# Optimization experiments

Hardware: AMD Instinct MI355X
Metric: run time of the kernel (lower is better)

## Reference

```python
import jax, jax.numpy as jnp
import numpy as np

C_Z = 128
C_H = 128
L = 512
EPS = 1e-5


def _layer_norm(x, w, b):
    mu = jnp.mean(x, axis=-1, keepdims=True)
    var = jnp.mean(jnp.square(x - mu), axis=-1, keepdims=True)
    return (x - mu) * jax.lax.rsqrt(var + EPS) * w + b


def setup_inputs() -> dict:
    key = jax.random.key(0)
    ks = jax.random.split(key, 10)
    s_z = 1.0 / np.sqrt(C_Z)
    s_h = 1.0 / np.sqrt(C_H)
    return {
        "z": jax.random.normal(ks[0], (L, L, C_Z), dtype=jnp.float32),
        "pair_mask": jax.random.randint(ks[1], (L, L), 0, 2, dtype=jnp.int32),
        "ln_in_w": jnp.ones((C_Z,), jnp.float32),
        "ln_in_b": jnp.zeros((C_Z,), jnp.float32),
        "ln_out_w": jnp.ones((C_H,), jnp.float32),
        "ln_out_b": jnp.zeros((C_H,), jnp.float32),
        # weights stored [in, out] so forward is x @ W
        "W_proj_a": jax.random.uniform(ks[2], (C_Z, C_H), jnp.float32, -s_z, s_z),
        "W_gate_a": jax.random.uniform(ks[3], (C_Z, C_H), jnp.float32, -s_z, s_z),
        "W_proj_b": jax.random.uniform(ks[4], (C_Z, C_H), jnp.float32, -s_z, s_z),
        "W_gate_b": jax.random.uniform(ks[5], (C_Z, C_H), jnp.float32, -s_z, s_z),
        "W_gate_out": jax.random.uniform(ks[6], (C_Z, C_Z), jnp.float32, -s_z, s_z),
        "W_proj_out": jax.random.uniform(ks[7], (C_H, C_Z), jnp.float32, -s_h, s_h),
    }


def reference(z, pair_mask, ln_in_w, ln_in_b, ln_out_w, ln_out_b,
              W_proj_a, W_gate_a, W_proj_b, W_gate_b, W_gate_out, W_proj_out):
    mask = pair_mask.astype(z.dtype)[..., None]  # [L, L, 1]
    z_ln = _layer_norm(z, ln_in_w, ln_in_b)      # [L, L, c_z]
    a = jax.nn.sigmoid(z_ln @ W_gate_a) * (z_ln @ W_proj_a) * mask  # [L, L, c_h]
    b = jax.nn.sigmoid(z_ln @ W_gate_b) * (z_ln @ W_proj_b) * mask  # [L, L, c_h]
    m = jnp.einsum('ikc,jkc->ijc', a, b)         # channel-batched matmul
    m_ln = _layer_norm(m, ln_out_w, ln_out_b)
    g = jax.nn.sigmoid(z_ln @ W_gate_out)        # [L, L, c_z]
    dz = g * (m_ln @ W_proj_out)
    return dz * mask
```

## Files before the change

kernel.cpp:

```cpp
#include <hip/hip_runtime.h>
#include <stdint.h>

#define LDIM 512
#define LLTOT 262144
#define EPSV 1e-5f

typedef short bf16x8 __attribute__((ext_vector_type(8)));
typedef float f32x4 __attribute__((ext_vector_type(4)));
typedef __attribute__((address_space(1))) unsigned as1_u32;
typedef __attribute__((address_space(3))) unsigned as3_u32;

__device__ __forceinline__ void stage16(const void* g, void* l) {
  __builtin_amdgcn_global_load_lds((as1_u32*)g, (as3_u32*)l, 16, 0, 0);
}

__device__ __forceinline__ unsigned short f2bf(float f) {
  union { float f; unsigned u; } v; v.f = f;
  unsigned r = v.u + 0x7FFFu + ((v.u >> 16) & 1u);
  return (unsigned short)(r >> 16);
}
__device__ __forceinline__ float bf2f(unsigned short h) {
  union { unsigned u; float f; } v; v.u = ((unsigned)h) << 16;
  return v.f;
}
__device__ __forceinline__ float sigm(float x) { return 1.0f / (1.0f + __expf(-x)); }


__global__ void k_prep(const float* __restrict__ Wpa, const float* __restrict__ Wga,
                       const float* __restrict__ Wpb, const float* __restrict__ Wgb,
                       const float* __restrict__ Wgo, const float* __restrict__ Wpo,
                       unsigned short* __restrict__ Wt) {
  int t = blockIdx.x * blockDim.x + threadIdx.x;
  int mat = t >> 14;
  int rem = t & 16383;
  int o = rem >> 7;
  int c = rem & 127;
  const float* src;
  switch (mat) {
    case 0: src = Wga; break;
    case 1: src = Wpa; break;
    case 2: src = Wgb; break;
    case 3: src = Wpb; break;
    case 4: src = Wgo; break;
    default: src = Wpo; break;
  }
  Wt[mat * 16384 + o * 128 + c] = f2bf(src[c * 128 + o]);
}

__global__ __launch_bounds__(256) void k_proj(const float* __restrict__ z,
                                              const float* __restrict__ lnw,
                                              const float* __restrict__ lnb,
                                              const unsigned short* __restrict__ Wt,
                                              const int* __restrict__ maskp,
                                              unsigned short* __restrict__ a_f,
                                              unsigned short* __restrict__ b_f,
                                              unsigned short* __restrict__ gout) {
  __shared__ __align__(16) unsigned char zbuf[128 * 272];
  __shared__ __align__(16) unsigned char stg[128 * 80];
  __shared__ float maskf[128];
  const int t = threadIdx.x;
  const int bid = blockIdx.x;
  const long r0 = (long)bid * 128;
  const int w = t >> 6, lane = t & 63;
  const int mn = lane & 15, q4 = lane >> 4;
  const int k0 = (bid & 3) * 128;
  const int i16 = bid >> 6;
  const int irem = (bid >> 2) & 15;

  if (t < 128) maskf[t] = (float)maskp[r0 + t];

  {
    const int half = lane >> 5, l32 = lane & 31;
    const float4 lwv = ((const float4*)lnw)[l32];
    const float4 lbv = ((const float4*)lnb)[l32];
#pragma unroll 4
    for (int rr = 0; rr < 32; rr += 2) {
      const int row = w * 32 + rr + half;
      float4 v = ((const float4*)(z + (r0 + row) * 128))[l32];
      float s = (v.x + v.y) + (v.z + v.w);
      float q = v.x * v.x + v.y * v.y + v.z * v.z + v.w * v.w;
#pragma unroll
      for (int off = 16; off; off >>= 1) { s += __shfl_xor(s, off); q += __shfl_xor(q, off); }
      float mu = s * (1.0f / 128.0f);
      float rs = rsqrtf(q * (1.0f / 128.0f) - mu * mu + EPSV);
      ushort4 o;
      o.x = f2bf((v.x - mu) * rs * lwv.x + lbv.x);
      o.y = f2bf((v.y - mu) * rs * lwv.y + lbv.y);
      o.z = f2bf((v.z - mu) * rs * lwv.z + lbv.z);
      o.w = f2bf((v.w - mu) * rs * lwv.w + lbv.w);
      *(ushort4*)(&zbuf[row * 272 + l32 * 8]) = o;
    }
  }
  __syncthreads();

  const int kcbase = k0 >> 5;
#pragma unroll 1
  for (int p = 0; p < 2; ++p) {
    const unsigned short* Wg = Wt + (p * 2) * 16384;
    const unsigned short* Wp = Wt + (p * 2 + 1) * 16384;
    unsigned short* dst = p ? b_f : a_f;
    bf16x8 wg[2][4], wp[2][4];
#pragma unroll
    for (int ntl = 0; ntl < 2; ++ntl)
#pragma unroll
      for (int kk = 0; kk < 4; ++kk) {
        const int o = (w * 2 + ntl) * 16 + mn;
        wg[ntl][kk] = *(const bf16x8*)(Wg + o * 128 + kk * 32 + q4 * 8);
        wp[ntl][kk] = *(const bf16x8*)(Wp + o * 128 + kk * 32 + q4 * 8);
      }
#pragma unroll 1
    for (int rg = 0; rg < 8; ++rg) {
      bf16x8 afr[4];
#pragma unroll
      for (int kk = 0; kk < 4; ++kk)
        afr[kk] = *(const bf16x8*)(&zbuf[(rg * 16 + mn) * 272 + kk * 64 + q4 * 16]);
      f32x4 aG[2] = {{0.f,0.f,0.f,0.f},{0.f,0.f,0.f,0.f}};
      f32x4 aP[2] = {{0.f,0.f,0.f,0.f},{0.f,0.f,0.f,0.f}};
#pragma unroll
      for (int kk = 0; kk < 4; ++kk)
#pragma unroll
        for (int ntl = 0; ntl < 2; ++ntl) {
          aG[ntl] = __builtin_amdgcn_mfma_f32_16x16x32_bf16(afr[kk], wg[ntl][kk], aG[ntl], 0, 0, 0);
          aP[ntl] = __builtin_amdgcn_mfma_f32_16x16x32_bf16(afr[kk], wp[ntl][kk], aP[ntl], 0, 0, 0);
        }
      const int rowb = rg * 16 + q4 * 4;
      const int kbyte = (rg & 1) * 32 + q4 * 8;
#pragma unroll
      for (int ntl = 0; ntl < 2; ++ntl) {
        const int c = (w * 2 + ntl) * 16 + mn;
        unsigned short hv[4];
#pragma unroll
        for (int r = 0; r < 4; ++r)
          hv[r] = f2bf(sigm(aG[ntl][r]) * aP[ntl][r] * maskf[rowb + r]);
        uint2 pk;
        pk.x = (unsigned)hv[0] | ((unsigned)hv[1] << 16);
        pk.y = (unsigned)hv[2] | ((unsigned)hv[3] << 16);
        *(uint2*)(&stg[c * 80 + kbyte]) = pk;
      }
      if (rg & 1) {
        __syncthreads();
        const int kc = kcbase + (rg >> 1);
        const int ch2 = t >> 1, off = (t & 1) * 32;
        char* d = (char*)dst + (long)ch2 * 524288 + (long)kc * 32768 +
                  i16 * 1024 + irem * 64 + off;
        const unsigned char* sp = &stg[ch2 * 80 + off];
        *(int4*)d = *(const int4*)sp;
        *(int4*)(d + 16) = *(const int4*)(sp + 16);
        __syncthreads();
      }
    }
  }

  {
    const unsigned short* Wgp = Wt + 4 * 16384;
    bf16x8 wg[2][4];
#pragma unroll
    for (int ntl = 0; ntl < 2; ++ntl)
#pragma unroll
      for (int kk = 0; kk < 4; ++kk)
        wg[ntl][kk] = *(const bf16x8*)(Wgp + ((w * 2 + ntl) * 16 + mn) * 128 + kk * 32 + q4 * 8);
#pragma unroll 1
    for (int rg = 0; rg < 8; ++rg) {
      bf16x8 afr[4];
#pragma unroll
      for (int kk = 0; kk < 4; ++kk)
        afr[kk] = *(const bf16x8*)(&zbuf[(rg * 16 + mn) * 272 + kk * 64 + q4 * 16]);
      f32x4 aG[2] = {{0.f,0.f,0.f,0.f},{0.f,0.f,0.f,0.f}};
#pragma unroll
      for (int kk = 0; kk < 4; ++kk)
#pragma unroll
        for (int ntl = 0; ntl < 2; ++ntl)
          aG[ntl] = __builtin_amdgcn_mfma_f32_16x16x32_bf16(afr[kk], wg[ntl][kk], aG[ntl], 0, 0, 0);
      const int rowb = rg * 16 + q4 * 4;
#pragma unroll
      for (int ntl = 0; ntl < 2; ++ntl) {
        const int c = (w * 2 + ntl) * 16 + mn;
#pragma unroll
        for (int r = 0; r < 4; ++r)
          gout[(r0 + rowb + r) * 128 + c] = f2bf(sigm(aG[ntl][r]));
      }
    }
  }
}

__global__ __launch_bounds__(256) void k_einsum(const unsigned short* __restrict__ af_g,
                                                const unsigned short* __restrict__ bf_g,
                                                unsigned short* __restrict__ m_t) {
  __shared__ __align__(16) unsigned char shm[36864];
  const int t = threadIdx.x;
  const int w = t >> 6, lane = t & 63;
  const int bid = blockIdx.x;
  const int xcd = bid & 7;
  const int j = bid >> 3;
  const int ch = xcd * 16 + (j >> 4);
  const int tile = j & 15;
  const int ti = tile >> 2, tj = tile & 3;
  const int wr = w >> 1, wc = w & 1;
  const int mn = lane & 15, q4 = lane >> 4;
  const int loff = (mn * 4 + q4) * 16;
  const long chbase = (long)ch * 524288;

  const char* gsrc[4];
#pragma unroll
  for (int u = 0; u < 4; ++u) {
    const int f = w * 4 + u;
    gsrc[u] = (f < 8)
        ? (const char*)af_g + chbase + (long)(ti * 8 + f) * 1024 + lane * 16
        : (const char*)bf_g + chbase + (long)(tj * 8 + (f - 8)) * 1024 + lane * 16;
  }

  f32x4 acc[4][4];
#pragma unroll
  for (int i = 0; i < 4; ++i)
#pragma unroll
    for (int jj = 0; jj < 4; ++jj) acc[i][jj] = (f32x4){0.f, 0.f, 0.f, 0.f};

#define STAGE(q, k32)                                                          \
  {                                                                            \
    _Pragma("unroll")                                                          \
    for (int u = 0; u < 4; ++u)                                                \
      stage16(gsrc[u] + (long)(k32) * 32768,                                   \
              &shm[(q) * 16384 + (w * 4 + u) * 1024]);                         \
  }

  int cur = 0;
  STAGE(0, 0)
  __syncthreads();
#pragma unroll 1
  for (int k32 = 0; k32 < 16; ++k32) {
    if (k32 < 15) STAGE(cur ^ 1, k32 + 1)
    bf16x8 afr[4], bfr[4];
#pragma unroll
    for (int mt = 0; mt < 4; ++mt)
      afr[mt] = *(const bf16x8*)(&shm[cur * 16384 + (wr * 4 + mt) * 1024 + loff]);
#pragma unroll
    for (int nt = 0; nt < 4; ++nt)
      bfr[nt] = *(const bf16x8*)(&shm[cur * 16384 + 8192 + (wc * 4 + nt) * 1024 + loff]);
#pragma unroll
    for (int mt = 0; mt < 4; ++mt)
#pragma unroll
      for (int nt = 0; nt < 4; ++nt)
        acc[mt][nt] = __builtin_amdgcn_mfma_f32_16x16x32_bf16(
            afr[mt], bfr[nt], acc[mt][nt], 0, 0, 0);
    __syncthreads();
    cur ^= 1;
  }
#undef STAGE

  unsigned char* eb = shm + w * 9216;
#pragma unroll
  for (int mt = 0; mt < 4; ++mt)
#pragma unroll
    for (int nt = 0; nt < 4; ++nt)
#pragma unroll
      for (int r = 0; r < 4; ++r) {
        int rl = mt * 16 + q4 * 4 + r;
        int cl = nt * 16 + mn;
        *(unsigned short*)(&eb[rl * 144 + cl * 2]) = f2bf(acc[mt][nt][r]);
      }
  char* Mg = (char*)m_t + (long)ch * 524288 +
             (long)(ti * 128 + wr * 64) * 1024 + (tj * 128 + wc * 64) * 2;
#pragma unroll
  for (int it = 0; it < 8; ++it) {
    int rl = it * 8 + (lane >> 3), cc = lane & 7;
    *(int4*)(Mg + (long)rl * 1024 + cc * 16) = *(const int4*)(&eb[rl * 144 + cc * 16]);
  }
}

__global__ __launch_bounds__(256) void k_out(const unsigned short* __restrict__ m_t,
                                             const unsigned short* __restrict__ gbuf,
                                             const unsigned short* __restrict__ Wt,
                                             const int* __restrict__ maskp,
                                             const float* __restrict__ lnw,
                                             const float* __restrict__ lnb,
                                             float* __restrict__ out) {
  __shared__ unsigned char mln[64 * 272];
  __shared__ float obuf[64 * 132];
  __shared__ float lw[128], lb[128], mk[64];
  const int t = threadIdx.x;
  const long r0 = (long)blockIdx.x * 64;

#pragma unroll
  for (int it = 0; it < 4; ++it) {
    int chunk = it * 256 + t;
    int c = chunk >> 3, cc = chunk & 7;
    int4 rv = *(const int4*)((const char*)m_t + (long)c * 524288 + r0 * 2 + cc * 16);
    const unsigned short* rp = (const unsigned short*)&rv;
#pragma unroll
    for (int e = 0; e < 8; ++e) {
      int er = (e + cc) & 7;
      *(unsigned short*)(&mln[(cc * 8 + er) * 272 + c * 2]) = rp[er];
    }
  }
  if (t < 128) { lw[t] = lnw[t]; lb[t] = lnb[t]; }
  if (t < 64) mk[t] = (float)maskp[r0 + t];
  __syncthreads();

  {
    int row = t >> 2, part = t & 3;
    float xv[32];
    float s = 0.f, q = 0.f;
#pragma unroll
    for (int jj = 0; jj < 16; ++jj) {
      unsigned u = *(const unsigned*)(&mln[row * 272 + part * 64 + jj * 4]);
      float x0 = bf2f((unsigned short)(u & 0xffff));
      float x1 = bf2f((unsigned short)(u >> 16));
      xv[2 * jj] = x0; xv[2 * jj + 1] = x1;
      s += x0 + x1; q += x0 * x0 + x1 * x1;
    }
    s += __shfl_xor(s, 1); q += __shfl_xor(q, 1);
    s += __shfl_xor(s, 2); q += __shfl_xor(q, 2);
    float mu = s * (1.f / 128.f);
    float var = q * (1.f / 128.f) - mu * mu;
    float rs = rsqrtf(var + EPSV);
#pragma unroll
    for (int jj = 0; jj < 16; ++jj) {
      int c = part * 32 + 2 * jj;
      unsigned short h0 = f2bf((xv[2 * jj] - mu) * rs * lw[c] + lb[c]);
      unsigned short h1 = f2bf((xv[2 * jj + 1] - mu) * rs * lw[c + 1] + lb[c + 1]);
      *(unsigned*)(&mln[row * 272 + c * 2]) = (unsigned)h0 | ((unsigned)h1 << 16);
    }
  }
  __syncthreads();

  const int w = t >> 6, lane = t & 63;
  const int mn = lane & 15, q4 = lane >> 4;
  bf16x8 afr[4];
#pragma unroll
  for (int kk = 0; kk < 4; ++kk)
    afr[kk] = *(const bf16x8*)(&mln[(w * 16 + mn) * 272 + kk * 64 + q4 * 16]);
  const unsigned short* Wp = Wt + 5 * 16384;
#pragma unroll 1
  for (int nt = 0; nt < 8; ++nt) {
    f32x4 acc = {0.f, 0.f, 0.f, 0.f};
#pragma unroll
    for (int kk = 0; kk < 4; ++kk) {
      bf16x8 bfr = *(const bf16x8*)(Wp + (nt * 16 + mn) * 128 + kk * 32 + q4 * 8);
      acc = __builtin_amdgcn_mfma_f32_16x16x32_bf16(afr[kk], bfr, acc, 0, 0, 0);
    }
    const int cl = nt * 16 + mn;
#pragma unroll
    for (int r = 0; r < 4; ++r)
      obuf[(w * 16 + q4 * 4 + r) * 132 + cl] = acc[r];
  }
  __syncthreads();

#pragma unroll
  for (int it = 0; it < 8; ++it) {
    int chunk = it * 256 + t;
    int row = chunk >> 5, cc = chunk & 31;
    float4 v = *(const float4*)(&obuf[row * 132 + cc * 4]);
    uint2 gp = *(const uint2*)((const char*)gbuf + (r0 + row) * 256 + cc * 8);
    float mval = mk[row];
    v.x *= bf2f((unsigned short)(gp.x & 0xffff)) * mval;
    v.y *= bf2f((unsigned short)(gp.x >> 16)) * mval;
    v.z *= bf2f((unsigned short)(gp.y & 0xffff)) * mval;
    v.w *= bf2f((unsigned short)(gp.y >> 16)) * mval;
    *(float4*)(out + (r0 + row) * 128 + cc * 4) = v;
  }
}

extern "C" void kernel_launch(void* const* d_in, const int* in_sizes, int n_in,
                              void* d_out, int out_size, void* d_ws, size_t ws_size,
                              hipStream_t stream) {
  const float* z    = (const float*)d_in[0];
  const int* maskp  = (const int*)d_in[1];
  const float* lniw = (const float*)d_in[2];
  const float* lnib = (const float*)d_in[3];
  const float* lnow = (const float*)d_in[4];
  const float* lnob = (const float*)d_in[5];
  const float* Wpa  = (const float*)d_in[6];
  const float* Wga  = (const float*)d_in[7];
  const float* Wpb  = (const float*)d_in[8];
  const float* Wgb  = (const float*)d_in[9];
  const float* Wgo  = (const float*)d_in[10];
  const float* Wpo  = (const float*)d_in[11];
  float* out = (float*)d_out;

  char* ws = (char*)d_ws;
  unsigned short* a_f = (unsigned short*)(ws);
  unsigned short* b_f = (unsigned short*)(ws + 67108864);
  unsigned short* g   = (unsigned short*)(ws + 134217728);
  unsigned short* m_t = (unsigned short*)(ws + 201326592);
  unsigned short* Wt  = (unsigned short*)(ws + 268435456);

  k_prep<<<384, 256, 0, stream>>>(Wpa, Wga, Wpb, Wgb, Wgo, Wpo, Wt);
  k_proj<<<2048, 256, 0, stream>>>(z, lniw, lnib, Wt, maskp, a_f, b_f, g);
  k_einsum<<<2048, 256, 0, stream>>>(a_f, b_f, m_t);
  k_out<<<4096, 256, 0, stream>>>(m_t, g, Wt, maskp, lnow, lnob, out);
}
```

Measured before the change: 507.0 us.

## Triple-buffer einsum staging, write projections directly, use hardware bf16 pack converts

The einsum k-loop moves from double to triple buffering in LDS. It uses explicit vmcnt waits plus a single barrier per iteration instead of two syncthreads, so global-to-LDS loads overlap more with MFMA work. k_proj drops the LDS staging buffer and its barriers and writes the gated projections straight to the blocked global layout as 8-byte stores. All software bf16 rounding is replaced by the v_cvt_pk_bf16_f32 instruction, and the input layernorm now handles 8 floats per lane. Risks are more LDS per einsum block, which may lower occupancy, and smaller, less coalesced global stores in k_proj.

```diff
diff --git a/kernel.cpp b/kernel.cpp
--- a/kernel.cpp
+++ b/kernel.cpp
@@ -22,6 +22,11 @@
 __device__ __forceinline__ float bf2f(unsigned short h) {
   union { unsigned u; float f; } v; v.u = ((unsigned)h) << 16;
   return v.f;
+}
+__device__ __forceinline__ unsigned cvtpk(float lo, float hi) {
+  unsigned r;
+  asm("v_cvt_pk_bf16_f32 %0, %1, %2" : "=v"(r) : "v"(lo), "v"(hi));
+  return r;
 }
 __device__ __forceinline__ float sigm(float x) { return 1.0f / (1.0f + __expf(-x)); }
 
@@ -56,7 +61,6 @@
                                               unsigned short* __restrict__ b_f,
                                               unsigned short* __restrict__ gout) {
   __shared__ __align__(16) unsigned char zbuf[128 * 272];
-  __shared__ __align__(16) unsigned char stg[128 * 80];
   __shared__ float maskf[128];
   const int t = threadIdx.x;
   const int bid = blockIdx.x;
@@ -70,30 +74,33 @@
   if (t < 128) maskf[t] = (float)maskp[r0 + t];
 
   {
-    const int half = lane >> 5, l32 = lane & 31;
-    const float4 lwv = ((const float4*)lnw)[l32];
-    const float4 lbv = ((const float4*)lnb)[l32];
-#pragma unroll 4
-    for (int rr = 0; rr < 32; rr += 2) {
-      const int row = w * 32 + rr + half;
-      float4 v = ((const float4*)(z + (r0 + row) * 128))[l32];
-      float s = (v.x + v.y) + (v.z + v.w);
-      float q = v.x * v.x + v.y * v.y + v.z * v.z + v.w * v.w;
-#pragma unroll
-      for (int off = 16; off; off >>= 1) { s += __shfl_xor(s, off); q += __shfl_xor(q, off); }
+    const int sub = lane >> 4, c16 = lane & 15;
+    const float4 lw0 = ((const float4*)lnw)[c16 * 2];
+    const float4 lw1 = ((const float4*)lnw)[c16 * 2 + 1];
+    const float4 lb0 = ((const float4*)lnb)[c16 * 2];
+    const float4 lb1 = ((const float4*)lnb)[c16 * 2 + 1];
+#pragma unroll 2
+    for (int rr = 0; rr < 8; ++rr) {
+      const int row = w * 32 + rr * 4 + sub;
+      const float4* zr = (const float4*)(z + (r0 + row) * 128);
+      float4 v0 = zr[c16 * 2], v1 = zr[c16 * 2 + 1];
+      float s = ((v0.x + v0.y) + (v0.z + v0.w)) + ((v1.x + v1.y) + (v1.z + v1.w));
+      float q = v0.x * v0.x + v0.y * v0.y + v0.z * v0.z + v0.w * v0.w +
+                v1.x * v1.x + v1.y * v1.y + v1.z * v1.z + v1.w * v1.w;
+#pragma unroll
+      for (int off = 8; off; off >>= 1) { s += __shfl_xor(s, off); q += __shfl_xor(q, off); }
       float mu = s * (1.0f / 128.0f);
       float rs = rsqrtf(q * (1.0f / 128.0f) - mu * mu + EPSV);
-      ushort4 o;
-      o.x = f2bf((v.x - mu) * rs * lwv.x + lbv.x);
-      o.y = f2bf((v.y - mu) * rs * lwv.y + lbv.y);
-      o.z = f2bf((v.z - mu) * rs * lwv.z + lbv.z);
-      o.w = f2bf((v.w - mu) * rs * lwv.w + lbv.w);
-      *(ushort4*)(&zbuf[row * 272 + l32 * 8]) = o;
-    }
-  }
-  __syncthreads();
-
-  const int kcbase = k0 >> 5;
+      uint4 o;
+      o.x = cvtpk((v0.x - mu) * rs * lw0.x + lb0.x, (v0.y - mu) * rs * lw0.y + lb0.y);
+      o.y = cvtpk((v0.z - mu) * rs * lw0.z + lb0.z, (v0.w - mu) * rs * lw0.w + lb0.w);
+      o.z = cvtpk((v1.x - mu) * rs * lw1.x + lb1.x, (v1.y - mu) * rs * lw1.y + lb1.y);
+      o.w = cvtpk((v1.z - mu) * rs * lw1.z + lb1.z, (v1.w - mu) * rs * lw1.w + lb1.w);
+      *(uint4*)(&zbuf[row * 272 + c16 * 16]) = o;
+    }
+  }
+  __syncthreads();
+
 #pragma unroll 1
   for (int p = 0; p < 2; ++p) {
     const unsigned short* Wg = Wt + (p * 2) * 16384;
@@ -124,29 +131,20 @@
           aP[ntl] = __builtin_amdgcn_mfma_f32_16x16x32_bf16(afr[kk], wp[ntl][kk], aP[ntl], 0, 0, 0);
         }
       const int rowb = rg * 16 + q4 * 4;
-      const int kbyte = (rg & 1) * 32 + q4 * 8;
+      const int kpos = k0 + rowb;
+      const int kc = kpos >> 5;
+      const int cell = (irem * 4 + ((kpos >> 3) & 3)) * 16 + (kpos & 7) * 2;
 #pragma unroll
       for (int ntl = 0; ntl < 2; ++ntl) {
         const int c = (w * 2 + ntl) * 16 + mn;
-        unsigned short hv[4];
-#pragma unroll
-        for (int r = 0; r < 4; ++r)
-          hv[r] = f2bf(sigm(aG[ntl][r]) * aP[ntl][r] * maskf[rowb + r]);
+        float e0 = sigm(aG[ntl][0]) * aP[ntl][0] * maskf[rowb + 0];
+        float e1 = sigm(aG[ntl][1]) * aP[ntl][1] * maskf[rowb + 1];
+        float e2 = sigm(aG[ntl][2]) * aP[ntl][2] * maskf[rowb + 2];
+        float e3 = sigm(aG[ntl][3]) * aP[ntl][3] * maskf[rowb + 3];
         uint2 pk;
-        pk.x = (unsigned)hv[0] | ((unsigned)hv[1] << 16);
-        pk.y = (unsigned)hv[2] | ((unsigned)hv[3] << 16);
-        *(uint2*)(&stg[c * 80 + kbyte]) = pk;
-      }
-      if (rg & 1) {
-        __syncthreads();
-        const int kc = kcbase + (rg >> 1);
-        const int ch2 = t >> 1, off = (t & 1) * 32;
-        char* d = (char*)dst + (long)ch2 * 524288 + (long)kc * 32768 +
-                  i16 * 1024 + irem * 64 + off;
-        const unsigned char* sp = &stg[ch2 * 80 + off];
-        *(int4*)d = *(const int4*)sp;
-        *(int4*)(d + 16) = *(const int4*)(sp + 16);
-        __syncthreads();
+        pk.x = cvtpk(e0, e1);
+        pk.y = cvtpk(e2, e3);
+        *(uint2*)((char*)dst + (long)c * 524288 + kc * 32768 + i16 * 1024 + cell) = pk;
       }
     }
   }
@@ -175,9 +173,12 @@
 #pragma unroll
       for (int ntl = 0; ntl < 2; ++ntl) {
         const int c = (w * 2 + ntl) * 16 + mn;
-#pragma unroll
-        for (int r = 0; r < 4; ++r)
-          gout[(r0 + rowb + r) * 128 + c] = f2bf(sigm(aG[ntl][r]));
+        unsigned u01 = cvtpk(sigm(aG[ntl][0]), sigm(aG[ntl][1]));
+        unsigned u23 = cvtpk(sigm(aG[ntl][2]), sigm(aG[ntl][3]));
+        gout[(r0 + rowb + 0) * 128 + c] = (unsigned short)u01;
+        gout[(r0 + rowb + 1) * 128 + c] = (unsigned short)(u01 >> 16);
+        gout[(r0 + rowb + 2) * 128 + c] = (unsigned short)u23;
+        gout[(r0 + rowb + 3) * 128 + c] = (unsigned short)(u23 >> 16);
       }
     }
   }
@@ -186,7 +187,7 @@
 __global__ __launch_bounds__(256) void k_einsum(const unsigned short* __restrict__ af_g,
                                                 const unsigned short* __restrict__ bf_g,
                                                 unsigned short* __restrict__ m_t) {
-  __shared__ __align__(16) unsigned char shm[36864];
+  __shared__ __align__(16) unsigned char shm[49152];
   const int t = threadIdx.x;
   const int w = t >> 6, lane = t & 63;
   const int bid = blockIdx.x;
@@ -223,41 +224,48 @@
               &shm[(q) * 16384 + (w * 4 + u) * 1024]);                         \
   }
 
-  int cur = 0;
   STAGE(0, 0)
-  __syncthreads();
+  STAGE(1, 1)
 #pragma unroll 1
   for (int k32 = 0; k32 < 16; ++k32) {
-    if (k32 < 15) STAGE(cur ^ 1, k32 + 1)
+    if (k32 < 15) {
+      asm volatile("s_waitcnt vmcnt(4)\n\ts_barrier" ::: "memory");
+    } else {
+      asm volatile("s_waitcnt vmcnt(0)\n\ts_barrier" ::: "memory");
+    }
+    if (k32 + 2 < 16) STAGE((k32 + 2) % 3, k32 + 2)
+    const int cb = (k32 % 3) * 16384;
     bf16x8 afr[4], bfr[4];
 #pragma unroll
     for (int mt = 0; mt < 4; ++mt)
-      afr[mt] = *(const bf16x8*)(&shm[cur * 16384 + (wr * 4 + mt) * 1024 + loff]);
+      afr[mt] = *(const bf16x8*)(&shm[cb + (wr * 4 + mt) * 1024 + loff]);
 #pragma unroll
     for (int nt = 0; nt < 4; ++nt)
-      bfr[nt] = *(const bf16x8*)(&shm[cur * 16384 + 8192 + (wc * 4 + nt) * 1024 + loff]);
+      bfr[nt] = *(const bf16x8*)(&shm[cb + 8192 + (wc * 4 + nt) * 1024 + loff]);
 #pragma unroll
     for (int mt = 0; mt < 4; ++mt)
 #pragma unroll
       for (int nt = 0; nt < 4; ++nt)
         acc[mt][nt] = __builtin_amdgcn_mfma_f32_16x16x32_bf16(
             afr[mt], bfr[nt], acc[mt][nt], 0, 0, 0);
-    __syncthreads();
-    cur ^= 1;
   }
 #undef STAGE
+  __syncthreads();
 
   unsigned char* eb = shm + w * 9216;
 #pragma unroll
   for (int mt = 0; mt < 4; ++mt)
 #pragma unroll
-    for (int nt = 0; nt < 4; ++nt)
-#pragma unroll
-      for (int r = 0; r < 4; ++r) {
-        int rl = mt * 16 + q4 * 4 + r;
-        int cl = nt * 16 + mn;
-        *(unsigned short*)(&eb[rl * 144 + cl * 2]) = f2bf(acc[mt][nt][r]);
-      }
+    for (int nt = 0; nt < 4; ++nt) {
+      const int rlb = mt * 16 + q4 * 4;
+      const int cl = nt * 16 + mn;
+      unsigned u01 = cvtpk(acc[mt][nt][0], acc[mt][nt][1]);
+      unsigned u23 = cvtpk(acc[mt][nt][2], acc[mt][nt][3]);
+      *(unsigned short*)(&eb[(rlb + 0) * 144 + cl * 2]) = (unsigned short)u01;
+      *(unsigned short*)(&eb[(rlb + 1) * 144 + cl * 2]) = (unsigned short)(u01 >> 16);
+      *(unsigned short*)(&eb[(rlb + 2) * 144 + cl * 2]) = (unsigned short)u23;
+      *(unsigned short*)(&eb[(rlb + 3) * 144 + cl * 2]) = (unsigned short)(u23 >> 16);
+    }
   char* Mg = (char*)m_t + (long)ch * 524288 +
              (long)(ti * 128 + wr * 64) * 1024 + (tj * 128 + wc * 64) * 2;
 #pragma unroll
@@ -316,9 +324,9 @@
 #pragma unroll
     for (int jj = 0; jj < 16; ++jj) {
       int c = part * 32 + 2 * jj;
-      unsigned short h0 = f2bf((xv[2 * jj] - mu) * rs * lw[c] + lb[c]);
-      unsigned short h1 = f2bf((xv[2 * jj + 1] - mu) * rs * lw[c + 1] + lb[c + 1]);
-      *(unsigned*)(&mln[row * 272 + c * 2]) = (unsigned)h0 | ((unsigned)h1 << 16);
+      unsigned pk = cvtpk((xv[2 * jj] - mu) * rs * lw[c] + lb[c],
+                          (xv[2 * jj + 1] - mu) * rs * lw[c + 1] + lb[c + 1]);
+      *(unsigned*)(&mln[row * 272 + c * 2]) = pk;
     }
   }
   __syncthreads();
```

Result: no change. 501.9 us (-1.0%).
